# Performance work log

Measured on AMD Instinct MI355X. Metric: run time of the kernel, lower is better.

## Reference

```python
import jax, jax.numpy as jnp
import numpy as np

B, N, F_IN, T = 16, 512, 32, 24
K, C_OUT = 3, 64


def setup_inputs() -> dict:
    key = jax.random.key(0)
    k1, k2, k3, k4 = jax.random.split(key, 4)
    X = jax.random.normal(k1, (B, N, F_IN, T), dtype=jnp.float32)
    s_a = jax.random.uniform(k2, (B, N, N), dtype=jnp.float32)
    cheb = jax.random.normal(k3, (K, N, N), dtype=jnp.float32)
    # Theta per nn.Parameter(K, c_in, c_out), kaiming-style scale
    Theta = jax.random.normal(k4, (K, F_IN, C_OUT), dtype=jnp.float32) * np.float32(np.sqrt(2.0 / F_IN))
    return {"X": X, "s_a": s_a, "cheb": cheb, "Theta": Theta}


def reference(X, s_a, cheb, Theta):
    # A[k,b,n,m] = T_k[n,m] * s_a[b,n,m]  (attention-masked Chebyshev polynomial)
    A = cheb[:, None, :, :] * s_a[None, :, :, :]  # [K,B,N,N]
    # torch: rhs = bmm(A.permute(0,2,1), X_t); out_t = sum_k rhs @ Theta_k
    # -> out[t,b,m,o] = sum_{k,n,f} A[k,b,n,m] * X[b,n,f,t] * Theta[k,f,o]
    out = jnp.einsum('kbnm,bnft,kfo->tbmo', A, X, Theta)  # [T,B,N,c_out]
    return jax.nn.relu(out)  # graph_conv_act_func == 'relu'
```

## Files before the change

kernel.cpp:

```cpp
#include <hip/hip_runtime.h>
#include <hip/hip_bf16.h>

#define B_ 16
#define N_ 512
#define F_ 32
#define T_ 24
#define K_ 3
#define C_ 64
#define FT_ 768
#define KF_ 96

typedef __attribute__((ext_vector_type(8))) short bf16x8;
typedef __attribute__((ext_vector_type(4))) float f32x4;

static __device__ __forceinline__ ushort f2b(float x) {
  uint u = __float_as_uint(x);
  return (ushort)((u + 0x7fffu + ((u >> 16) & 1u)) >> 16);
}
static __device__ __forceinline__ uint pk2(float a, float b) {
  return (uint)f2b(a) | ((uint)f2b(b) << 16);
}

#define GLOAD_LDS16(g, l)                                                     \
  __builtin_amdgcn_global_load_lds(                                           \
      (const __attribute__((address_space(1))) void*)(g),                     \
      (__attribute__((address_space(3))) void*)(l), 16, 0, 0)


#define XP_PAD 260
__global__ __launch_bounds__(256) void prepX(const float* __restrict__ X,
                                             ushort* __restrict__ Xt2) {
  __shared__ ushort L[32 * XP_PAD];
  const int b = blockIdx.y;
  const int n0 = (blockIdx.x & 15) * 32;
  const int fg = blockIdx.x >> 4;
  const int tid = threadIdx.x;

  const float* Xp = X + ((size_t)b * N_ + n0) * FT_ + fg * 8;
#pragma unroll
  for (int it = 0; it < 8; ++it) {
    int c = tid + it * 256;
    int row = c >> 6, rem = c & 63;
    int f = rem >> 1, half = rem & 1;
    float4 v = *(const float4*)(Xp + (size_t)row * FT_ + f * 24 + half * 4);
    uint2 p; p.x = pk2(v.x, v.y); p.y = pk2(v.z, v.w);
    *(uint2*)&L[row * XP_PAD + f * 8 + half * 4] = p;
  }
  __syncthreads();
  const int ft2 = fg * 256 + tid;
  const int f = tid & 31, dt = tid >> 5;
  ushort a[32];
#pragma unroll
  for (int r = 0; r < 32; ++r) a[r] = L[r * XP_PAD + f * 8 + dt];
  uint w[16];
#pragma unroll
  for (int q = 0; q < 16; ++q) w[q] = (uint)a[2 * q] | ((uint)a[2 * q + 1] << 16);
  ushort* op = Xt2 + ((size_t)b * FT_ + ft2) * N_ + n0;
#pragma unroll
  for (int q = 0; q < 4; ++q) {
    uint4 v; v.x = w[4*q]; v.y = w[4*q+1]; v.z = w[4*q+2]; v.w = w[4*q+3];
    *((uint4*)op + q) = v;
  }
}

__global__ __launch_bounds__(256) void prepA(const float* __restrict__ SA,
                                             const float* __restrict__ CH,
                                             ushort* __restrict__ At) {
  const int kb = blockIdx.y;
  const int k = kb >> 4, b = kb & 15;
  const int m0 = (blockIdx.x & 7) * 64, n0 = (blockIdx.x >> 3) * 64;
  const int tid = threadIdx.x;
  const int ml = (tid & 15) * 4, nl = (tid >> 4) * 4;

  const float* cp = CH + ((size_t)k * N_ + n0 + nl) * N_ + m0 + ml;
  const float* sp = SA + ((size_t)b * N_ + n0 + nl) * N_ + m0 + ml;
  float4 p[4];
#pragma unroll
  for (int q = 0; q < 4; ++q) {
    float4 c = *(const float4*)(cp + (size_t)q * N_);
    float4 s = *(const float4*)(sp + (size_t)q * N_);
    p[q] = make_float4(c.x * s.x, c.y * s.y, c.z * s.z, c.w * s.w);
  }
  ushort* ob = At + (size_t)kb * N_ * N_ + (size_t)(m0 + ml) * N_ + n0 + nl;
#pragma unroll
  for (int s = 0; s < 4; ++s) {
    uint2 w;
    w.x = pk2(((const float*)&p[0])[s], ((const float*)&p[1])[s]);
    w.y = pk2(((const float*)&p[2])[s], ((const float*)&p[3])[s]);
    *(uint2*)(ob + (size_t)s * N_) = w;
  }
}

__global__ __launch_bounds__(256, 2) void stage1(const ushort* __restrict__ Xt2,
                                                 const ushort* __restrict__ At,
                                                 ushort* __restrict__ R2) {
  __shared__ __align__(16) ushort Abuf[2][128 * 64];
  __shared__ __align__(16) ushort Bbuf[2][128 * 64];
  const int kb = blockIdx.y;
  const int k = kb >> 4, b = kb & 15;
  const int ft0 = (blockIdx.x >> 2) * 128;
  const int m0 = (blockIdx.x & 3) * 128;
  const int tid = threadIdx.x, lane = tid & 63, wid = tid >> 6;
  const int wft = (wid >> 1) * 64, wm = (wid & 1) * 64;

  const char* Xbase = (const char*)(Xt2 + ((size_t)b * FT_ + ft0) * N_);
  const char* Bbase = (const char*)(At + ((size_t)kb * N_ + m0) * N_);
  const int srow = lane >> 3;
  const int scolS = ((lane & 7) * 16) ^ (srow << 4);

  f32x4 acc[4][4];
#pragma unroll
  for (int i = 0; i < 4; ++i)
#pragma unroll
    for (int j = 0; j < 4; ++j) acc[i][j] = (f32x4){0.f, 0.f, 0.f, 0.f};

#define STAGE1_LOAD(bufi, nb)                                                  \
  {                                                                            \
    _Pragma("unroll")                                                          \
    for (int c = 0; c < 4; ++c) {                                              \
      const int s = wid * 4 + c;                                               \
      const size_t go = (size_t)(s * 8 + srow) * 1024 + (nb) * 128 + scolS;    \
      GLOAD_LDS16(Xbase + go, (char*)Abuf[bufi] + s * 1024);                   \
      GLOAD_LDS16(Bbase + go, (char*)Bbuf[bufi] + s * 1024);                   \
    }                                                                          \
  }

  STAGE1_LOAD(0, 0);
  __syncthreads();

  int cur = 0;
  for (int nb = 0; nb < 8; ++nb) {
    if (nb < 7) STAGE1_LOAD(cur ^ 1, nb + 1);
    const char* Ab = (const char*)Abuf[cur];
    const char* Bb = (const char*)Bbuf[cur];
#pragma unroll
    for (int kk = 0; kk < 2; ++kk) {
      const int cb = (kk * 64 + (lane >> 4) * 16) ^ ((lane & 7) << 4);
      bf16x8 af[4], bfv[4];
#pragma unroll
      for (int i = 0; i < 4; ++i)
        af[i] = *(const bf16x8*)(Ab + (wft + i * 16 + (lane & 15)) * 128 + cb);
#pragma unroll
      for (int j = 0; j < 4; ++j)
        bfv[j] = *(const bf16x8*)(Bb + (wm + j * 16 + (lane & 15)) * 128 + cb);
#pragma unroll
      for (int i = 0; i < 4; ++i)
#pragma unroll
        for (int j = 0; j < 4; ++j)
          acc[i][j] = __builtin_amdgcn_mfma_f32_16x16x32_bf16(af[i], bfv[j], acc[i][j], 0, 0, 0);
    }
    __syncthreads();
    cur ^= 1;
  }

  const int col = lane & 15, rg4 = (lane >> 4) * 4;
#pragma unroll
  for (int i = 0; i < 4; ++i) {
    const int ft2 = ft0 + wft + i * 16 + rg4;
    const int t = ft2 >> 5, f = ft2 & 31;
#pragma unroll
    for (int j = 0; j < 4; ++j) {
      const int m = m0 + wm + j * 16 + col;
      uint2 w;
      w.x = pk2(acc[i][j][0], acc[i][j][1]);
      w.y = pk2(acc[i][j][2], acc[i][j][3]);
      *(uint2*)(R2 + ((size_t)(b * T_ + t) * N_ + m) * KF_ + k * 32 + f) = w;
    }
  }
}

__global__ __launch_bounds__(256, 2) void stage2(const ushort* __restrict__ R2,
                                                 const float* __restrict__ TH,
                                                 float* __restrict__ Out) {
  const int mh = blockIdx.x;
  const int t = blockIdx.y, b = blockIdx.z;
  const int tid = threadIdx.x, lane = tid & 63, wid = tid >> 6;
  const int m0w = mh * 256 + wid * 64;
  const int col = lane & 15, kc = (lane >> 4) * 8, rg4 = (lane >> 4) * 4;

  bf16x8 bfr[3][4];
#pragma unroll
  for (int ks = 0; ks < 3; ++ks)
#pragma unroll
    for (int j = 0; j < 4; ++j) {
      const float* tp = TH + (size_t)(ks * 32 + kc) * C_ + j * 16 + col;
      bf16x8 v;
#pragma unroll
      for (int q = 0; q < 8; ++q) v[q] = (short)f2b(tp[(size_t)q * C_]);
      bfr[ks][j] = v;
    }

  const ushort* Rb = R2 + ((size_t)b * T_ + t) * N_ * KF_;
  float* Ob = Out + ((size_t)t * B_ + b) * N_ * C_;

#pragma unroll
  for (int i = 0; i < 4; ++i) {
    const int m = m0w + i * 16;
    bf16x8 af[3];
#pragma unroll
    for (int ks = 0; ks < 3; ++ks)
      af[ks] = *(const bf16x8*)(Rb + (size_t)(m + col) * KF_ + ks * 32 + kc);
    f32x4 acc[4];
#pragma unroll
    for (int j = 0; j < 4; ++j) acc[j] = (f32x4){0.f, 0.f, 0.f, 0.f};
#pragma unroll
    for (int ks = 0; ks < 3; ++ks)
#pragma unroll
      for (int j = 0; j < 4; ++j)
        acc[j] = __builtin_amdgcn_mfma_f32_16x16x32_bf16(af[ks], bfr[ks][j], acc[j], 0, 0, 0);
#pragma unroll
    for (int j = 0; j < 4; ++j)
#pragma unroll
      for (int r = 0; r < 4; ++r)
        Ob[(size_t)(m + rg4 + r) * C_ + j * 16 + col] = fmaxf(acc[j][r], 0.f);
  }
}

extern "C" void kernel_launch(void* const* d_in, const int* in_sizes, int n_in,
                              void* d_out, int out_size, void* d_ws, size_t ws_size,
                              hipStream_t stream) {
  const float* X  = (const float*)d_in[0];
  const float* SA = (const float*)d_in[1];
  const float* CH = (const float*)d_in[2];
  const float* TH = (const float*)d_in[3];
  float* Out = (float*)d_out;

  char* ws = (char*)d_ws;
  ushort* R2  = (ushort*)(ws);
  ushort* Xt2 = (ushort*)(ws + 37748736);
  ushort* At  = (ushort*)(ws + 37748736 + 12582912);

  prepX<<<dim3(48, 16), 256, 0, stream>>>(X, Xt2);
  prepA<<<dim3(64, 48), 256, 0, stream>>>(SA, CH, At);
  stage1<<<dim3(24, 48), 256, 0, stream>>>(Xt2, At, R2);
  stage2<<<dim3(2, 24, 16), 256, 0, stream>>>(R2, TH, Out);
}
```

Baseline: 162.7 us.

## Merge prep kernels, share X tile across all K in stage1, repack R2 layout

Fuses prepX and prepA into a single launch, with each A block now handling four tiles. Stage1 is restructured so that one block computes all three Chebyshev orders for a 128x64 tile. The X tile is loaded once and reused across K, which cuts X global traffic. The double buffering is dropped in favour of single-buffered loads with two barriers per step, the block IDs are swizzled for locality, and occupancy is raised to 3. R2 is repacked into an 8-element-chunk layout so the stage1 stores and stage2 loads are contiguous, at the cost of losing load/compute overlap.

```diff
diff --git a/kernel.cpp b/kernel.cpp
--- a/kernel.cpp
+++ b/kernel.cpp
@@ -26,147 +26,162 @@
       (const __attribute__((address_space(1))) void*)(g),                     \
       (__attribute__((address_space(3))) void*)(l), 16, 0, 0)
 
-
 #define XP_PAD 260
-__global__ __launch_bounds__(256) void prepX(const float* __restrict__ X,
-                                             ushort* __restrict__ Xt2) {
+__global__ __launch_bounds__(256) void prep(const float* __restrict__ X,
+                                            const float* __restrict__ SA,
+                                            const float* __restrict__ CH,
+                                            ushort* __restrict__ Xt2,
+                                            ushort* __restrict__ At) {
   __shared__ ushort L[32 * XP_PAD];
-  const int b = blockIdx.y;
-  const int n0 = (blockIdx.x & 15) * 32;
-  const int fg = blockIdx.x >> 4;
+  const int bid = blockIdx.x;
   const int tid = threadIdx.x;
-
-  const float* Xp = X + ((size_t)b * N_ + n0) * FT_ + fg * 8;
-#pragma unroll
-  for (int it = 0; it < 8; ++it) {
-    int c = tid + it * 256;
-    int row = c >> 6, rem = c & 63;
-    int f = rem >> 1, half = rem & 1;
-    float4 v = *(const float4*)(Xp + (size_t)row * FT_ + f * 24 + half * 4);
-    uint2 p; p.x = pk2(v.x, v.y); p.y = pk2(v.z, v.w);
-    *(uint2*)&L[row * XP_PAD + f * 8 + half * 4] = p;
+  if (bid < 768) {
+    const int local = bid % 48;
+    const int b = bid / 48;
+    const int n0 = (local & 15) * 32;
+    const int fg = local >> 4;
+    const float* Xp = X + ((size_t)b * N_ + n0) * FT_ + fg * 8;
+#pragma unroll
+    for (int it = 0; it < 8; ++it) {
+      int c = tid + it * 256;
+      int row = c >> 6, rem = c & 63;
+      int f = rem >> 1, half = rem & 1;
+      float4 v = *(const float4*)(Xp + (size_t)row * FT_ + f * 24 + half * 4);
+      uint2 p; p.x = pk2(v.x, v.y); p.y = pk2(v.z, v.w);
+      *(uint2*)&L[row * XP_PAD + f * 8 + half * 4] = p;
+    }
+    __syncthreads();
+    const int ft2 = fg * 256 + tid;
+    const int f = tid & 31, dt = tid >> 5;
+    ushort a[32];
+#pragma unroll
+    for (int r = 0; r < 32; ++r) a[r] = L[r * XP_PAD + f * 8 + dt];
+    uint w[16];
+#pragma unroll
+    for (int q = 0; q < 16; ++q) w[q] = (uint)a[2 * q] | ((uint)a[2 * q + 1] << 16);
+    ushort* op = Xt2 + ((size_t)b * FT_ + ft2) * N_ + n0;
+#pragma unroll
+    for (int q = 0; q < 4; ++q) {
+      uint4 v; v.x = w[4*q]; v.y = w[4*q+1]; v.z = w[4*q+2]; v.w = w[4*q+3];
+      *((uint4*)op + q) = v;
+    }
+  } else {
+    const int a = bid - 768;
+    const int kb = a >> 4;
+    const int k = kb >> 4, b = kb & 15;
+    const int sub = a & 15;
+    const int ml = (tid & 15) * 4, nl = (tid >> 4) * 4;
+#pragma unroll
+    for (int c = 0; c < 4; ++c) {
+      const int tile = sub * 4 + c;
+      const int m0 = (tile & 7) * 64, n0 = (tile >> 3) * 64;
+      const float* cp = CH + ((size_t)k * N_ + n0 + nl) * N_ + m0 + ml;
+      const float* sp = SA + ((size_t)b * N_ + n0 + nl) * N_ + m0 + ml;
+      float4 p[4];
+#pragma unroll
+      for (int q = 0; q < 4; ++q) {
+        float4 cv = *(const float4*)(cp + (size_t)q * N_);
+        float4 sv = *(const float4*)(sp + (size_t)q * N_);
+        p[q] = make_float4(cv.x * sv.x, cv.y * sv.y, cv.z * sv.z, cv.w * sv.w);
+      }
+      ushort* ob = At + (size_t)kb * N_ * N_ + (size_t)(m0 + ml) * N_ + n0 + nl;
+#pragma unroll
+      for (int s = 0; s < 4; ++s) {
+        uint2 w;
+        w.x = pk2(((const float*)&p[0])[s], ((const float*)&p[1])[s]);
+        w.y = pk2(((const float*)&p[2])[s], ((const float*)&p[3])[s]);
+        *(uint2*)(ob + (size_t)s * N_) = w;
+      }
+    }
   }
-  __syncthreads();
-  const int ft2 = fg * 256 + tid;
-  const int f = tid & 31, dt = tid >> 5;
-  ushort a[32];
-#pragma unroll
-  for (int r = 0; r < 32; ++r) a[r] = L[r * XP_PAD + f * 8 + dt];
-  uint w[16];
-#pragma unroll
-  for (int q = 0; q < 16; ++q) w[q] = (uint)a[2 * q] | ((uint)a[2 * q + 1] << 16);
-  ushort* op = Xt2 + ((size_t)b * FT_ + ft2) * N_ + n0;
-#pragma unroll
-  for (int q = 0; q < 4; ++q) {
-    uint4 v; v.x = w[4*q]; v.y = w[4*q+1]; v.z = w[4*q+2]; v.w = w[4*q+3];
-    *((uint4*)op + q) = v;
-  }
-}
-
-__global__ __launch_bounds__(256) void prepA(const float* __restrict__ SA,
-                                             const float* __restrict__ CH,
-                                             ushort* __restrict__ At) {
-  const int kb = blockIdx.y;
-  const int k = kb >> 4, b = kb & 15;
-  const int m0 = (blockIdx.x & 7) * 64, n0 = (blockIdx.x >> 3) * 64;
-  const int tid = threadIdx.x;
-  const int ml = (tid & 15) * 4, nl = (tid >> 4) * 4;
-
-  const float* cp = CH + ((size_t)k * N_ + n0 + nl) * N_ + m0 + ml;
-  const float* sp = SA + ((size_t)b * N_ + n0 + nl) * N_ + m0 + ml;
-  float4 p[4];
-#pragma unroll
-  for (int q = 0; q < 4; ++q) {
-    float4 c = *(const float4*)(cp + (size_t)q * N_);
-    float4 s = *(const float4*)(sp + (size_t)q * N_);
-    p[q] = make_float4(c.x * s.x, c.y * s.y, c.z * s.z, c.w * s.w);
-  }
-  ushort* ob = At + (size_t)kb * N_ * N_ + (size_t)(m0 + ml) * N_ + n0 + nl;
-#pragma unroll
-  for (int s = 0; s < 4; ++s) {
-    uint2 w;
-    w.x = pk2(((const float*)&p[0])[s], ((const float*)&p[1])[s]);
-    w.y = pk2(((const float*)&p[2])[s], ((const float*)&p[3])[s]);
-    *(uint2*)(ob + (size_t)s * N_) = w;
-  }
-}
-
-__global__ __launch_bounds__(256, 2) void stage1(const ushort* __restrict__ Xt2,
+}
+
+__global__ __launch_bounds__(256, 3) void stage1(const ushort* __restrict__ Xt2,
                                                  const ushort* __restrict__ At,
                                                  ushort* __restrict__ R2) {
-  __shared__ __align__(16) ushort Abuf[2][128 * 64];
-  __shared__ __align__(16) ushort Bbuf[2][128 * 64];
-  const int kb = blockIdx.y;
-  const int k = kb >> 4, b = kb & 15;
-  const int ft0 = (blockIdx.x >> 2) * 128;
-  const int m0 = (blockIdx.x & 3) * 128;
+  __shared__ __align__(16) ushort Abuf[128 * 64];
+  __shared__ __align__(16) ushort Bbuf[3][64 * 64];
+
+  const int bid = blockIdx.x;
+  const int logical = (bid & 7) * 96 + (bid >> 3);
+  const int b = logical / 48;
+  const int tile = logical % 48;
+  const int ft0 = (tile >> 3) * 128;
+  const int m0 = (tile & 7) * 64;
   const int tid = threadIdx.x, lane = tid & 63, wid = tid >> 6;
-  const int wft = (wid >> 1) * 64, wm = (wid & 1) * 64;
-
-  const char* Xbase = (const char*)(Xt2 + ((size_t)b * FT_ + ft0) * N_);
-  const char* Bbase = (const char*)(At + ((size_t)kb * N_ + m0) * N_);
+  const int wft = (wid >> 1) * 64, wm = (wid & 1) * 32;
   const int srow = lane >> 3;
   const int scolS = ((lane & 7) * 16) ^ (srow << 4);
 
-  f32x4 acc[4][4];
-#pragma unroll
-  for (int i = 0; i < 4; ++i)
-#pragma unroll
-    for (int j = 0; j < 4; ++j) acc[i][j] = (f32x4){0.f, 0.f, 0.f, 0.f};
-
-#define STAGE1_LOAD(bufi, nb)                                                  \
-  {                                                                            \
-    _Pragma("unroll")                                                          \
-    for (int c = 0; c < 4; ++c) {                                              \
-      const int s = wid * 4 + c;                                               \
-      const size_t go = (size_t)(s * 8 + srow) * 1024 + (nb) * 128 + scolS;    \
-      GLOAD_LDS16(Xbase + go, (char*)Abuf[bufi] + s * 1024);                   \
-      GLOAD_LDS16(Bbase + go, (char*)Bbuf[bufi] + s * 1024);                   \
-    }                                                                          \
-  }
-
-  STAGE1_LOAD(0, 0);
-  __syncthreads();
-
-  int cur = 0;
+  const char* Xbase = (const char*)(Xt2 + ((size_t)b * FT_ + ft0) * N_);
+  const char* Bk[3];
+#pragma unroll
+  for (int kq = 0; kq < 3; ++kq)
+    Bk[kq] = (const char*)(At + ((size_t)(kq * 16 + b) * N_ + m0) * N_);
+
+  f32x4 acc[3][4][2];
+#pragma unroll
+  for (int kq = 0; kq < 3; ++kq)
+#pragma unroll
+    for (int i = 0; i < 4; ++i)
+#pragma unroll
+      for (int j = 0; j < 2; ++j) acc[kq][i][j] = (f32x4){0.f, 0.f, 0.f, 0.f};
+
   for (int nb = 0; nb < 8; ++nb) {
-    if (nb < 7) STAGE1_LOAD(cur ^ 1, nb + 1);
-    const char* Ab = (const char*)Abuf[cur];
-    const char* Bb = (const char*)Bbuf[cur];
+    __syncthreads();
+#pragma unroll
+    for (int c = 0; c < 4; ++c) {
+      const int s = wid * 4 + c;
+      const size_t go = (size_t)(s * 8 + srow) * 1024 + nb * 128 + scolS;
+      GLOAD_LDS16(Xbase + go, (char*)Abuf + s * 1024);
+    }
+#pragma unroll
+    for (int c = 0; c < 6; ++c) {
+      const int idx = wid * 6 + c;
+      const int kq = idx >> 3, seg = idx & 7;
+      const size_t go = (size_t)(seg * 8 + srow) * 1024 + nb * 128 + scolS;
+      GLOAD_LDS16(Bk[kq] + go, (char*)Bbuf[kq] + seg * 1024);
+    }
+    __syncthreads();
 #pragma unroll
     for (int kk = 0; kk < 2; ++kk) {
       const int cb = (kk * 64 + (lane >> 4) * 16) ^ ((lane & 7) << 4);
-      bf16x8 af[4], bfv[4];
+      bf16x8 af[4];
 #pragma unroll
       for (int i = 0; i < 4; ++i)
-        af[i] = *(const bf16x8*)(Ab + (wft + i * 16 + (lane & 15)) * 128 + cb);
-#pragma unroll
-      for (int j = 0; j < 4; ++j)
-        bfv[j] = *(const bf16x8*)(Bb + (wm + j * 16 + (lane & 15)) * 128 + cb);
-#pragma unroll
-      for (int i = 0; i < 4; ++i)
-#pragma unroll
-        for (int j = 0; j < 4; ++j)
-          acc[i][j] = __builtin_amdgcn_mfma_f32_16x16x32_bf16(af[i], bfv[j], acc[i][j], 0, 0, 0);
-    }
-    __syncthreads();
-    cur ^= 1;
+        af[i] = *(const bf16x8*)((const char*)Abuf + (wft + i * 16 + (lane & 15)) * 128 + cb);
+#pragma unroll
+      for (int kq = 0; kq < 3; ++kq) {
+        bf16x8 bf[2];
+#pragma unroll
+        for (int j = 0; j < 2; ++j)
+          bf[j] = *(const bf16x8*)((const char*)Bbuf[kq] + (wm + j * 16 + (lane & 15)) * 128 + cb);
+#pragma unroll
+        for (int i = 0; i < 4; ++i)
+#pragma unroll
+          for (int j = 0; j < 2; ++j)
+            acc[kq][i][j] = __builtin_amdgcn_mfma_f32_16x16x32_bf16(af[i], bf[j], acc[kq][i][j], 0, 0, 0);
+      }
+    }
   }
 
   const int col = lane & 15, rg4 = (lane >> 4) * 4;
 #pragma unroll
-  for (int i = 0; i < 4; ++i) {
-    const int ft2 = ft0 + wft + i * 16 + rg4;
-    const int t = ft2 >> 5, f = ft2 & 31;
-#pragma unroll
-    for (int j = 0; j < 4; ++j) {
-      const int m = m0 + wm + j * 16 + col;
-      uint2 w;
-      w.x = pk2(acc[i][j][0], acc[i][j][1]);
-      w.y = pk2(acc[i][j][2], acc[i][j][3]);
-      *(uint2*)(R2 + ((size_t)(b * T_ + t) * N_ + m) * KF_ + k * 32 + f) = w;
-    }
-  }
+  for (int kq = 0; kq < 3; ++kq)
+#pragma unroll
+    for (int i = 0; i < 4; ++i) {
+      const int ft2 = ft0 + wft + i * 16 + rg4;
+      const int t = ft2 >> 5, f = ft2 & 31;
+      const size_t rowbase = ((size_t)(b * T_ + t) * 12 + kq * 4 + (f >> 3)) * 4096 + (f & 7);
+#pragma unroll
+      for (int j = 0; j < 2; ++j) {
+        const int m = m0 + wm + j * 16 + col;
+        uint2 w;
+        w.x = pk2(acc[kq][i][j][0], acc[kq][i][j][1]);
+        w.y = pk2(acc[kq][i][j][2], acc[kq][i][j][3]);
+        *(uint2*)(R2 + rowbase + (size_t)m * 8) = w;
+      }
+    }
 }
 
 __global__ __launch_bounds__(256, 2) void stage2(const ushort* __restrict__ R2,
@@ -176,21 +191,21 @@
   const int t = blockIdx.y, b = blockIdx.z;
   const int tid = threadIdx.x, lane = tid & 63, wid = tid >> 6;
   const int m0w = mh * 256 + wid * 64;
-  const int col = lane & 15, kc = (lane >> 4) * 8, rg4 = (lane >> 4) * 4;
+  const int col = lane & 15, g = lane >> 4, rg4 = g * 4;
 
   bf16x8 bfr[3][4];
 #pragma unroll
   for (int ks = 0; ks < 3; ++ks)
 #pragma unroll
     for (int j = 0; j < 4; ++j) {
-      const float* tp = TH + (size_t)(ks * 32 + kc) * C_ + j * 16 + col;
+      const float* tp = TH + (size_t)(ks * 32 + g * 8) * C_ + j * 16 + col;
       bf16x8 v;
 #pragma unroll
       for (int q = 0; q < 8; ++q) v[q] = (short)f2b(tp[(size_t)q * C_]);
       bfr[ks][j] = v;
     }
 
-  const ushort* Rb = R2 + ((size_t)b * T_ + t) * N_ * KF_;
+  const ushort* Rb = R2 + ((size_t)(b * T_ + t) * 12) * 4096;
   float* Ob = Out + ((size_t)t * B_ + b) * N_ * C_;
 
 #pragma unroll
@@ -199,7 +214,7 @@
     bf16x8 af[3];
 #pragma unroll
     for (int ks = 0; ks < 3; ++ks)
-      af[ks] = *(const bf16x8*)(Rb + (size_t)(m + col) * KF_ + ks * 32 + kc);
+      af[ks] = *(const bf16x8*)(Rb + (size_t)(ks * 4 + g) * 4096 + (size_t)(m + col) * 8);
     f32x4 acc[4];
 #pragma unroll
     for (int j = 0; j < 4; ++j) acc[j] = (f32x4){0.f, 0.f, 0.f, 0.f};
@@ -230,8 +245,7 @@
   ushort* Xt2 = (ushort*)(ws + 37748736);
   ushort* At  = (ushort*)(ws + 37748736 + 12582912);
 
-  prepX<<<dim3(48, 16), 256, 0, stream>>>(X, Xt2);
-  prepA<<<dim3(64, 48), 256, 0, stream>>>(SA, CH, At);
-  stage1<<<dim3(24, 48), 256, 0, stream>>>(Xt2, At, R2);
+  prep<<<dim3(1536), 256, 0, stream>>>(X, SA, CH, Xt2, At);
+  stage1<<<dim3(768), 256, 0, stream>>>(Xt2, At, R2);
   stage2<<<dim3(2, 24, 16), 256, 0, stream>>>(R2, TH, Out);
 }
```

After: 145.5 us. 1.12x faster.
